# Optimization experiments

Measured on AMD Instinct MI355X. Metric: run time of the kernel, lower is better.

Reference implementation:

```python
import jax, jax.numpy as jnp
import numpy as np

SIGMA2_MU = 0.5  # hyper_params['sigma2_mu']
R = 128          # number of spatial basis functions
NV = 2000        # number of query points
KM1 = 30         # K - 1


def setup_inputs() -> dict:
    key = jax.random.key(0)
    k1, k2, k3, k4 = jax.random.split(key, 4)
    Xi_evals = jax.random.normal(k1, (R, NV), dtype=jnp.float32)
    vec_W_post_mean = jax.random.normal(k2, (R * KM1, 1), dtype=jnp.float32)
    vec_W_post_cov = jax.random.normal(k3, (R * KM1, R * KM1), dtype=jnp.float32)
    C_mu = jax.random.normal(k4, (NV, 1), dtype=jnp.float32)
    return {"Xi_evals": Xi_evals, "vec_W_post_mean": vec_W_post_mean,
            "vec_W_post_cov": vec_W_post_cov, "C_mu": C_mu}


def reference(Xi_evals, vec_W_post_mean, vec_W_post_cov, C_mu):
    # Xi_evals: (r, Nv); vec_W_post_mean: (r*(K-1), 1); vec_W_post_cov: (r*(K-1), r*(K-1))
    r, Nv = Xi_evals.shape
    Km1 = vec_W_post_mean.shape[0] // r
    K = Km1 + 1
    X = Xi_evals.T                                # (Nv, r)
    # kron(x^T, I_{K-1}) @ w  ==  X @ W  with W = w.reshape(r, K-1)
    W = vec_W_post_mean.reshape(r, Km1)
    Post_mean_c = X @ W                           # (Nv, K-1)
    # kron(x^T, I) @ Cov @ kron(x, I): quadratic form over r-blocks
    C4 = vec_W_post_cov.reshape(r, Km1, r, Km1)   # (i, k, j, l)
    A = jnp.einsum('vi,ikjl->vkjl', X, C4)        # (Nv, K-1, r, K-1)
    Post_cov_c = jnp.einsum('vkjl,vj->vkl', A, X) # (Nv, K-1, K-1)
    Post_mean_coefs = jnp.concatenate([C_mu, Post_mean_c], axis=1)  # (Nv, K)
    Post_cov_mats = jnp.zeros((Nv, K, K), dtype=Xi_evals.dtype)
    Post_cov_mats = Post_cov_mats.at[:, 0, 0].set(SIGMA2_MU)
    Post_cov_mats = Post_cov_mats.at[:, 1:, 1:].set(Post_cov_c)
    return Post_mean_coefs, Post_cov_mats
```

## Files before the change

kernel.cpp:

```cpp
#include <hip/hip_runtime.h>

typedef _Float16 f16;
typedef _Float16 f16x8 __attribute__((ext_vector_type(8)));
typedef float    f32x16 __attribute__((ext_vector_type(16)));

#define NV      2000
#define RR      128
#define KM1     30
#define KKOUT   31
#define NQ      900
#define QQ      961
#define COV_OFF 62000

#define B5_BYTES 17104896
#define XH_BYTES 524288

#define PERM_BLKS  3840
#define XC1_BLKS   128
#define ZERO_BLKS  1877
#define MEAN_BLKS  248
#define PREP_GRID  (PERM_BLKS + XC1_BLKS + ZERO_BLKS + MEAN_BLKS)

__global__ void prep_kernel(const float* __restrict__ Xi,
                            const float* __restrict__ Wm,
                            const float* __restrict__ cov,
                            const float* __restrict__ Cmu,
                            f16* __restrict__ B5,
                            f16* __restrict__ Xh,
                            float* __restrict__ outm,
                            float* __restrict__ oc) {
    __shared__ float rowS[3840];
    int b = blockIdx.x, tid = threadIdx.x;
    if (b < PERM_BLKS) {
        int i = b / 30, k = b - i * 30;
        int g = i >> 4;
        int j0 = g << 4;
        int W = 128 - j0;
        int lo = (i - j0) * 30;
        const float* src = cov + (size_t)b * 3840 + j0 * 30;
        for (int t = tid; t < W * 30; t += 256)
            rowS[t] = (t >= lo) ? src[t] : 0.f;
        __syncthreads();
        int n2 = (127 - i) * 15;
        for (int idx = tid; idx < n2; idx += 256) {
            int j = i + 1 + idx / 15;
            int p = idx - (j - i - 1) * 15;
            const float2 v2 = *(const float2*)(cov + (size_t)(j * 30 + k) * 3840 + i * 30 + 2 * p);
            rowS[(j - j0) * 30 + 2 * p]     += v2.x;
            rowS[(j - j0) * 30 + 2 * p + 1] += v2.y;
        }
        __syncthreads();
        int t_st = i & 15;
        int nOct = W >> 3;
        for (int it = tid; it < nOct * 30; it += 256) {
            int oct = it / 30, l = it - oct * 30;
            int j = j0 + oct * 8;
            int s = j >> 4, kq = (j >> 3) & 1;
            int q = k * 30 + l, qt = q >> 5, l31 = q & 31;
            int kz, slot;
            if (g < 4) { kz = g;     slot = s - g; }
            else       { kz = 7 - g; slot = s + 1; }
            f16 vals[8];
#pragma unroll
            for (int d = 0; d < 8; ++d) vals[d] = (f16)rowS[(j + d - j0) * 30 + l];
            f16* dst = B5 + ((((size_t)(qt * 4 + kz) * 16 + t_st) * 9 + slot) << 9)
                          + (kq * 32 + l31) * 8;
            *(uint4*)dst = *(uint4*)vals;
        }
        return;
    }
    b -= PERM_BLKS;
    if (b < XC1_BLKS) {
        int t = b * 256 + tid;
        int v = t & 2047, rc = t >> 11;
        f16 vals[8];
#pragma unroll
        for (int d = 0; d < 8; ++d) {
            float x = (v < NV) ? Xi[(rc * 8 + d) * NV + v] : 0.f;
            vals[d] = (f16)x;
        }
        *(uint4*)(Xh + (size_t)v * 128 + rc * 8) = *(uint4*)vals;
        return;
    }
    b -= XC1_BLKS;
    if (b < ZERO_BLKS) {
        size_t idx = ((size_t)b * 256 + tid) * 4;
        if (idx < (size_t)NV * QQ) {
            unsigned rem = (unsigned)(idx % QQ);
            float4 zv;
            zv.x = (rem == 0u)   ? 0.5f : 0.f;
            zv.y = (rem == 960u) ? 0.5f : 0.f;
            zv.z = (rem == 959u) ? 0.5f : 0.f;
            zv.w = (rem == 958u) ? 0.5f : 0.f;
            *(float4*)(oc + idx) = zv;
        }
        return;
    }
    b -= ZERO_BLKS;
    int t2 = b * 256 + tid;
    int c = t2 >> 11, v = t2 & 2047;
    if (v >= NV || c >= KKOUT) return;
    if (c == 0) { outm[(size_t)v * KKOUT] = Cmu[v]; return; }
    float acc = 0.f;
    const float* w = Wm + (c - 1);
#pragma unroll 8
    for (int i = 0; i < RR; ++i)
        acc = fmaf(Xi[i * NV + v], w[i * KM1], acc);
    outm[(size_t)v * KKOUT + c] = acc;
}

__device__ __forceinline__ void load9(f16x8 (&b)[9], const f16* p) {
#pragma unroll
    for (int m = 0; m < 9; ++m)
        b[m] = *(const f16x8*)(p + m * 512);
}

template<int KZ>
__device__ __forceinline__ void stage_compute(int t, int l31,
                                              const f16x8 (&bv)[9],
                                              const f16x8 (&xj)[2][8],
                                              f32x16 (&acc)[2]) {
    constexpr int NA = 8 - KZ, NB = 1 + KZ;
    const int srcl = l31 + ((t >> 3) << 5);
    f16 xA[2], xB[2];
#pragma unroll
    for (int fm = 0; fm < 2; ++fm) {
        unsigned short ha = __builtin_bit_cast(unsigned short, (f16)xj[fm][KZ][t & 7]);
        unsigned short hb = __builtin_bit_cast(unsigned short, (f16)xj[fm][7 - KZ][t & 7]);
        int pa = __shfl((int)ha, srcl, 64);
        int pb = __shfl((int)hb, srcl, 64);
        xA[fm] = __builtin_bit_cast(f16, (unsigned short)pa);
        xB[fm] = __builtin_bit_cast(f16, (unsigned short)pb);
    }
#pragma unroll
    for (int m = 0; m < NA; ++m)
#pragma unroll
        for (int fm = 0; fm < 2; ++fm)
            acc[fm] = __builtin_amdgcn_mfma_f32_32x32x16_f16(xj[fm][KZ + m] * xA[fm], bv[m], acc[fm], 0, 0, 0);
#pragma unroll
    for (int m2 = 0; m2 < NB; ++m2)
#pragma unroll
        for (int fm = 0; fm < 2; ++fm)
            acc[fm] = __builtin_amdgcn_mfma_f32_32x32x16_f16(xj[fm][7 - KZ + m2] * xB[fm], bv[NA + m2], acc[fm], 0, 0, 0);
}

template<int KZ>
__device__ __forceinline__ void kz_section(const f16*& gs,
                                           f16x8 (&cur)[9], f16x8 (&nxt)[9],
                                           const f16x8 (&xj)[2][8],
                                           f32x16 (&acc)[2], int l31) {
#pragma unroll
    for (int tt = 0; tt < 8; ++tt) {
        load9(nxt, gs); gs += 4608;
        stage_compute<KZ>(2 * tt, l31, cur, xj, acc);
        load9(cur, gs); gs += 4608;
        stage_compute<KZ>(2 * tt + 1, l31, nxt, xj, acc);
    }
}

__launch_bounds__(256, 1)
__global__ void gemm6_kernel(const f16* __restrict__ B5,
                             const f16* __restrict__ Xh,
                             float* __restrict__ out_cov) {
    const int bid = blockIdx.x;
    const int p = (bid & 7) * 29 + (bid >> 3);
    const int qt = p >> 3, y = p & 7;
    const int tid = threadIdx.x, lane = tid & 63, w = tid >> 6;
    const int l31 = lane & 31, kq = lane >> 5;
    const int v0 = y * 256 + w * 64;
    const int vr = v0 + l31;

    f16x8 xj[2][8];
#pragma unroll
    for (int fm = 0; fm < 2; ++fm)
#pragma unroll
        for (int u = 0; u < 8; ++u)
            xj[fm][u] = *(const f16x8*)(Xh + (size_t)(vr + fm * 32) * 128 + u * 16 + kq * 8);

    const f16* gbase = B5 + (size_t)qt * 64 * 4608 + lane * 8;

    f16x8 cur[9], nxt[9];
    load9(cur, gbase);
    const f16* gs = gbase + 4608;

    f32x16 acc[2] = {};
    kz_section<0>(gs, cur, nxt, xj, acc, l31);
    kz_section<1>(gs, cur, nxt, xj, acc, l31);
    kz_section<2>(gs, cur, nxt, xj, acc, l31);
    kz_section<3>(gs, cur, nxt, xj, acc, l31);

    const int q = qt * 32 + l31;
    if (q >= NQ) return;
    const int kk = q / 30, ll = q - kk * 30;
    float* cb = out_cov + (kk + 1) * KKOUT + (ll + 1);
#pragma unroll
    for (int fm = 0; fm < 2; ++fm) {
        int vb = v0 + fm * 32 + 4 * kq;
#pragma unroll
        for (int r = 0; r < 16; ++r) {
            int v = vb + (r & 3) + 8 * (r >> 2);
            if (v < NV) cb[(size_t)v * QQ] = acc[fm][r];
        }
    }
}

extern "C" void kernel_launch(void* const* d_in, const int* in_sizes, int n_in,
                              void* d_out, int out_size, void* d_ws, size_t ws_size,
                              hipStream_t stream) {
    const float* Xi  = (const float*)d_in[0];
    const float* Wm  = (const float*)d_in[1];
    const float* Cov = (const float*)d_in[2];
    const float* Cmu = (const float*)d_in[3];
    float* out      = (float*)d_out;
    float* out_mean = out;
    float* out_cov  = out + COV_OFF;
    f16* B5 = (f16*)d_ws;
    f16* Xh = (f16*)((char*)d_ws + B5_BYTES);

    prep_kernel <<<PREP_GRID, 256, 0, stream>>>(Xi, Wm, Cov, Cmu, B5, Xh,
                                                out_mean, out_cov);
    gemm6_kernel<<<232, 256, 0, stream>>>(B5, Xh, out_cov);
}
```

Measured before the change: 155.6 us.

## Split GEMM reduction across two blocks with atomic accumulation and triple-buffered loads

Splits the 64-stage reduction of each output tile into two halves, handled by separate blocks, which doubles the grid to 464 blocks and lets two blocks run per CU. The partial sums are combined with atomicAdd into the output, relying on the prep kernel having already zeroed it. The load pipeline also moves from double to triple buffering, unrolled at compile time through templates. The aim is better CU occupancy and latency hiding on 256 CUs. In exchange it adds atomic traffic, register pressure from the third buffer under the 2-blocks-per-CU bound, and a summation order that is no longer fixed.

```diff
diff --git a/kernel.cpp b/kernel.cpp
--- a/kernel.cpp
+++ b/kernel.cpp
@@ -115,18 +115,18 @@
         b[m] = *(const f16x8*)(p + m * 512);
 }
 
-template<int KZ>
-__device__ __forceinline__ void stage_compute(int t, int l31,
+template<int KZ, int T>
+__device__ __forceinline__ void stage_compute(int l31,
                                               const f16x8 (&bv)[9],
                                               const f16x8 (&xj)[2][8],
                                               f32x16 (&acc)[2]) {
     constexpr int NA = 8 - KZ, NB = 1 + KZ;
-    const int srcl = l31 + ((t >> 3) << 5);
+    const int srcl = l31 + ((T >> 3) << 5);
     f16 xA[2], xB[2];
 #pragma unroll
     for (int fm = 0; fm < 2; ++fm) {
-        unsigned short ha = __builtin_bit_cast(unsigned short, (f16)xj[fm][KZ][t & 7]);
-        unsigned short hb = __builtin_bit_cast(unsigned short, (f16)xj[fm][7 - KZ][t & 7]);
+        unsigned short ha = __builtin_bit_cast(unsigned short, (f16)xj[fm][KZ][T & 7]);
+        unsigned short hb = __builtin_bit_cast(unsigned short, (f16)xj[fm][7 - KZ][T & 7]);
         int pa = __shfl((int)ha, srcl, 64);
         int pb = __shfl((int)hb, srcl, 64);
         xA[fm] = __builtin_bit_cast(f16, (unsigned short)pa);
@@ -144,27 +144,33 @@
             acc[fm] = __builtin_amdgcn_mfma_f32_32x32x16_f16(xj[fm][7 - KZ + m2] * xB[fm], bv[NA + m2], acc[fm], 0, 0, 0);
 }
 
-template<int KZ>
-__device__ __forceinline__ void kz_section(const f16*& gs,
-                                           f16x8 (&cur)[9], f16x8 (&nxt)[9],
-                                           const f16x8 (&xj)[2][8],
-                                           f32x16 (&acc)[2], int l31) {
-#pragma unroll
-    for (int tt = 0; tt < 8; ++tt) {
-        load9(nxt, gs); gs += 4608;
-        stage_compute<KZ>(2 * tt, l31, cur, xj, acc);
-        load9(cur, gs); gs += 4608;
-        stage_compute<KZ>(2 * tt + 1, l31, nxt, xj, acc);
-    }
-}
-
-__launch_bounds__(256, 1)
-__global__ void gemm6_kernel(const f16* __restrict__ B5,
+template<int KZH, int ST>
+struct Stage {
+    static __device__ __forceinline__ void run(const f16* gs, f16x8 (&buf)[3][9],
+                                               const f16x8 (&xj)[2][8],
+                                               f32x16 (&acc)[2], int l31) {
+        if constexpr (ST + 2 < 32)
+            load9(buf[(ST + 2) % 3], gs + (size_t)(ST + 2) * 4608);
+        stage_compute<KZH * 2 + (ST >> 4), ST & 15>(l31, buf[ST % 3], xj, acc);
+        Stage<KZH, ST + 1>::run(gs, buf, xj, acc, l31);
+    }
+};
+template<int KZH>
+struct Stage<KZH, 32> {
+    static __device__ __forceinline__ void run(const f16*, f16x8 (&)[3][9],
+                                               const f16x8 (&)[2][8],
+                                               f32x16 (&)[2], int) {}
+};
+
+__launch_bounds__(256, 2)
+__global__ void gemm7_kernel(const f16* __restrict__ B5,
                              const f16* __restrict__ Xh,
                              float* __restrict__ out_cov) {
     const int bid = blockIdx.x;
-    const int p = (bid & 7) * 29 + (bid >> 3);
-    const int qt = p >> 3, y = p & 7;
+    const int p = (bid & 7) * 58 + (bid >> 3);
+    const int qt = p >> 4;
+    const int r  = p & 15;
+    const int y = r >> 1, h = r & 1;
     const int tid = threadIdx.x, lane = tid & 63, w = tid >> 6;
     const int l31 = lane & 31, kq = lane >> 5;
     const int v0 = y * 256 + w * 64;
@@ -177,17 +183,15 @@
         for (int u = 0; u < 8; ++u)
             xj[fm][u] = *(const f16x8*)(Xh + (size_t)(vr + fm * 32) * 128 + u * 16 + kq * 8);
 
-    const f16* gbase = B5 + (size_t)qt * 64 * 4608 + lane * 8;
-
-    f16x8 cur[9], nxt[9];
-    load9(cur, gbase);
-    const f16* gs = gbase + 4608;
+    const f16* gbase = B5 + ((size_t)qt * 64 + (size_t)h * 32) * 4608 + lane * 8;
+
+    f16x8 buf[3][9];
+    load9(buf[0], gbase);
+    load9(buf[1], gbase + 4608);
 
     f32x16 acc[2] = {};
-    kz_section<0>(gs, cur, nxt, xj, acc, l31);
-    kz_section<1>(gs, cur, nxt, xj, acc, l31);
-    kz_section<2>(gs, cur, nxt, xj, acc, l31);
-    kz_section<3>(gs, cur, nxt, xj, acc, l31);
+    if (h == 0) Stage<0, 0>::run(gbase, buf, xj, acc, l31);
+    else        Stage<1, 0>::run(gbase, buf, xj, acc, l31);
 
     const int q = qt * 32 + l31;
     if (q >= NQ) return;
@@ -197,9 +201,9 @@
     for (int fm = 0; fm < 2; ++fm) {
         int vb = v0 + fm * 32 + 4 * kq;
 #pragma unroll
-        for (int r = 0; r < 16; ++r) {
-            int v = vb + (r & 3) + 8 * (r >> 2);
-            if (v < NV) cb[(size_t)v * QQ] = acc[fm][r];
+        for (int rr = 0; rr < 16; ++rr) {
+            int v = vb + (rr & 3) + 8 * (rr >> 2);
+            if (v < NV) atomicAdd(cb + (size_t)v * QQ, acc[fm][rr]);
         }
     }
 }
@@ -219,5 +223,5 @@
 
     prep_kernel <<<PREP_GRID, 256, 0, stream>>>(Xi, Wm, Cov, Cmu, B5, Xh,
                                                 out_mean, out_cov);
-    gemm6_kernel<<<232, 256, 0, stream>>>(B5, Xh, out_cov);
-}
+    gemm7_kernel<<<464, 256, 0, stream>>>(B5, Xh, out_cov);
+}
```

Result: slower. 161.9 us (+4.0%).
